# Kernel tuning notes

Measured on AMD Instinct MI355X. Metric: run time of the kernel, lower is better.

Reference implementation:

```python
import jax, jax.numpy as jnp
import numpy as np

N, K, C, G = 100000, 16, 64, 8
EPS = 1e-5


def bn(x, gamma, beta):
    # training-mode BatchNorm1d over all dims except channel (last)
    axes = tuple(range(x.ndim - 1))
    m = jnp.mean(x, axis=axes)
    v = jnp.var(x, axis=axes)
    return (x - m) * jax.lax.rsqrt(v + EPS) * gamma + beta


def setup_inputs() -> dict:
    key = jax.random.key(0)
    ks = jax.random.split(key, 16)

    def lin(k, i, o):
        return (jax.random.normal(k, (i, o), jnp.float32) / np.sqrt(i)).astype(jnp.float32)

    feat = jax.random.normal(ks[0], (N, C), jnp.float32)
    coord = jax.random.uniform(ks[1], (N, 3), jnp.float32) * 10.0
    ref = jax.random.randint(ks[2], (N, K), 0, N)
    drop = jax.random.uniform(ks[3], (N, K)) < 0.05  # some padded (-1) neighbors
    ref = jnp.where(drop, -1, ref)

    return {
        "feat": feat, "coord": coord, "reference_index": ref,
        "wq": lin(ks[4], C, C), "bq": jnp.zeros((C,), jnp.float32),
        "gq": jnp.ones((C,), jnp.float32), "betaq": jnp.zeros((C,), jnp.float32),
        "wk": lin(ks[5], C, C), "bk": jnp.zeros((C,), jnp.float32),
        "gk": jnp.ones((C,), jnp.float32), "betak": jnp.zeros((C,), jnp.float32),
        "wv": lin(ks[6], C, C), "bv": jnp.zeros((C,), jnp.float32),
        "wp1": lin(ks[7], 3, C), "bp1": jnp.zeros((C,), jnp.float32),
        "gp": jnp.ones((C,), jnp.float32), "betap": jnp.zeros((C,), jnp.float32),
        "wp2": lin(ks[8], C, C), "bp2": jnp.zeros((C,), jnp.float32),
        "ww1": lin(ks[9], C, G), "bw1": jnp.zeros((G,), jnp.float32),
        "gw": jnp.ones((G,), jnp.float32), "betaw": jnp.zeros((G,), jnp.float32),
        "ww2": lin(ks[10], G, G), "bw2": jnp.zeros((G,), jnp.float32),
    }


def reference(feat, coord, reference_index,
              wq, bq, gq, betaq,
              wk, bk, gk, betak,
              wv, bv,
              wp1, bp1, gp, betap,
              wp2, bp2,
              ww1, bw1, gw, betaw,
              ww2, bw2):
    # q/k/v projections
    q = jax.nn.relu(bn(feat @ wq + bq, gq, betaq))   # [N, C]
    k = jax.nn.relu(bn(feat @ wk + bk, gk, betak))   # [N, C]
    v = feat @ wv + bv                                # [N, C]

    idx = jnp.clip(reference_index, 0, N - 1)         # clipped gather index [N, K]
    mask = (reference_index >= 0).astype(feat.dtype)  # sign(ref + 1)

    key_n = k[idx]                                    # [N, K, C] neighbor keys
    val = v[idx]                                      # [N, K, C]
    pos = coord[idx] - coord[:, None, :]              # [N, K, 3] relative coords

    relation_qk = key_n - q[:, None, :]               # [N, K, C]

    # pe_bias branch
    peb = jax.nn.relu(bn(pos @ wp1 + bp1, gp, betap)) @ wp2 + bp2  # [N, K, C]
    relation_qk = relation_qk + peb
    val = val + peb

    # weight encoding -> grouped softmax over neighbors, masked
    w = jax.nn.relu(bn(relation_qk @ ww1 + bw1, gw, betaw)) @ ww2 + bw2  # [N, K, G]
    w = jax.nn.softmax(w, axis=1) * mask[:, :, None]

    val = val.reshape(N, K, G, C // G)
    out = jnp.einsum('nsgi,nsg->ngi', val, w).reshape(N, C)
    return out
```

## Files before the change

### kernel.cpp

```cpp
#include <hip/hip_runtime.h>
#include <hip/hip_bf16.h>

#define NPTS 100000
#define KNBR 16
#define CCH  64
#define GRP  8
#define BN_EPS 1e-5f
#define NROW (NPTS * KNBR)
#define NBATCH (NROW / 64)
#define NPB   ((NPTS + 63) / 64)

#define O_QLINH 0
#define O_KLINH (NPTS * 32)
#define O_VLINH (NPTS * 64)
#define O_STAT  (NPTS * 96)
#define O_AFF   (O_STAT + 416)
#define O_W2W1  (O_AFF + 416)
#define O_BW1E  (O_W2W1 + 512)
#define O_QW1   (O_BW1E + 8)
#define O_KW1   (O_QW1 + NPTS * 8)

typedef __attribute__((ext_vector_type(8))) short short8;
typedef __attribute__((ext_vector_type(4))) short short4v;
typedef __attribute__((ext_vector_type(4))) float f32x4;
#define MFMA16(a, b, c) __builtin_amdgcn_mfma_f32_16x16x32_bf16(a, b, c, 0, 0, 0)

__device__ __forceinline__ int clip_idx(int r) {
    int i = r < 0 ? 0 : r;
    return i >= NPTS ? NPTS - 1 : i;
}
__device__ __forceinline__ unsigned short f2bf(float x) {
    union { float f; unsigned u; } v; v.f = x;
    unsigned r = v.u + 0x7fffu + ((v.u >> 16) & 1u);
    return (unsigned short)(r >> 16);
}
__device__ __forceinline__ float bf2f(unsigned short h) {
    union { unsigned u; float f; } v; v.u = ((unsigned)h) << 16;
    return v.f;
}
__device__ __forceinline__ unsigned pk_bf16(float lo, float hi) {
    unsigned r;
    asm("v_cvt_pk_bf16_f32 %0, %1, %2" : "=v"(r) : "v"(lo), "v"(hi));
    return r;
}
__device__ __forceinline__ int physK(int s) {
    return (s >> 5) * 32 + ((s >> 2) & 3) * 8 + ((s >> 4) & 1) * 4 + (s & 3);
}
__device__ __forceinline__ int aOff(int r, int p) {
    return r * 64 + (((p >> 3) ^ (r & 7)) << 3) + (p & 7);
}
__device__ __forceinline__ int kib_of(int i, int q) {
    return (i < 4) ? (4 * q + i) : (16 + 4 * q + (i - 4));
}

__global__ __launch_bounds__(512) void k_prep(
    const float* __restrict__ wp2, const float* __restrict__ ww1,
    const float* __restrict__ bw1, const float* __restrict__ bp2,
    float* __restrict__ stat, float* __restrict__ w2w1, float* __restrict__ bw1e)
{
    int t = threadIdx.x;
    if (t < 416) stat[t] = 0.f;
    int j = t >> 3, g = t & 7;
    float acc = 0.f;
    #pragma unroll 16
    for (int c = 0; c < 64; ++c) acc = fmaf(wp2[j * 64 + c], ww1[c * 8 + g], acc);
    w2w1[t] = acc;
    if (t < 8) {
        float b = bw1[t];
        #pragma unroll 16
        for (int c = 0; c < 64; ++c) b = fmaf(bp2[c], ww1[c * 8 + t], b);
        bw1e[t] = b;
    }
}

#define QKV_BLOCKS 512
__global__ __launch_bounds__(256) void k_qkv(
    const float* __restrict__ feat,
    const float* __restrict__ wq, const float* __restrict__ bq,
    const float* __restrict__ wk, const float* __restrict__ bk,
    const float* __restrict__ wv, const float* __restrict__ bv,
    const float* __restrict__ bp2,
    const float* __restrict__ coord, const int* __restrict__ ref,
    short* __restrict__ QlinH, short* __restrict__ KlinH, short* __restrict__ VlinH,
    float* __restrict__ stat)
{
    __shared__ short sA[4096];
    __shared__ float s_red[9];
    const int tid = threadIdx.x, lane = tid & 63, w = tid >> 6;
    const int q = lane >> 4, c15 = lane & 15;

    if (blockIdx.x >= QKV_BLOCKS) {
        float m[9];
        #pragma unroll
        for (int i = 0; i < 9; ++i) m[i] = 0.f;
        const int gid = (blockIdx.x - QKV_BLOCKS) * 256 + tid;
        const int stride = 128 * 256;
        for (int row = gid; row < NROW; row += stride) {
            int n = row >> 4;
            int idx = clip_idx(ref[row]);
            float px = coord[idx * 3 + 0] - coord[n * 3 + 0];
            float py = coord[idx * 3 + 1] - coord[n * 3 + 1];
            float pz = coord[idx * 3 + 2] - coord[n * 3 + 2];
            m[0] += px; m[1] += py; m[2] += pz;
            m[3] = fmaf(px, px, m[3]); m[4] = fmaf(py, py, m[4]); m[5] = fmaf(pz, pz, m[5]);
            m[6] = fmaf(px, py, m[6]); m[7] = fmaf(px, pz, m[7]); m[8] = fmaf(py, pz, m[8]);
        }
        if (tid < 9) s_red[tid] = 0.f;
        __syncthreads();
        #pragma unroll
        for (int off = 32; off >= 1; off >>= 1) {
            #pragma unroll
            for (int i = 0; i < 9; ++i) m[i] += __shfl_xor(m[i], off, 64);
        }
        if (lane == 0) {
            #pragma unroll
            for (int i = 0; i < 9; ++i) atomicAdd(&s_red[i], m[i]);
        }
        __syncthreads();
        if (tid < 9) atomicAdd(&stat[256 + tid], s_red[tid]);
        return;
    }

    short8 bfrag[3][2];
    float bias[3];
    #pragma unroll
    for (int t = 0; t < 3; ++t) {
        int gt = w * 3 + t;
        const float* W = (gt < 4) ? wq : (gt < 8) ? wk : wv;
        const float* B = (gt < 4) ? bq : (gt < 8) ? bk : bv;
        int col = (gt * 16 + c15) & 63;
        bias[t] = B[col] + (gt >= 8 ? bp2[col] : 0.f);
        #pragma unroll
        for (int kt = 0; kt < 2; ++kt) {
            short8 bb;
            #pragma unroll
            for (int i = 0; i < 8; ++i) {
                int kk = kt * 32 + kib_of(i, q);
                bb[i] = (short)f2bf(W[kk * 64 + col]);
            }
            bfrag[t][kt] = bb;
        }
    }
    float st_s[3], st_q[3];
    #pragma unroll
    for (int t = 0; t < 3; ++t) { st_s[t] = 0.f; st_q[t] = 0.f; }

    const int c4 = c15 * 4;
    const int pk4 = physK(c4);

    for (int b = blockIdx.x; b < NPB; b += QKV_BLOCKS) {
        const int pbase = b * 64;
        #pragma unroll
        for (int i = 0; i < 4; ++i) {
            int p = w * 16 + i * 4 + q;
            int n = pbase + p;
            float4 v = make_float4(0.f, 0.f, 0.f, 0.f);
            if (n < NPTS) v = *(const float4*)(feat + n * 64 + c4);
            short4v h;
            h[0] = (short)f2bf(v.x); h[1] = (short)f2bf(v.y);
            h[2] = (short)f2bf(v.z); h[3] = (short)f2bf(v.w);
            *(short4v*)(sA + aOff(p, pk4)) = h;
        }
        __syncthreads();
        #pragma unroll
        for (int mt = 0; mt < 4; ++mt) {
            int r = mt * 16 + c15;
            int ch0 = q ^ (r & 7);
            int ch1 = (4 + q) ^ (r & 7);
            short8 a0 = *(const short8*)(sA + r * 64 + (ch0 << 3));
            short8 a1 = *(const short8*)(sA + r * 64 + (ch1 << 3));
            #pragma unroll
            for (int t = 0; t < 3; ++t) {
                f32x4 acc = (f32x4){0.f, 0.f, 0.f, 0.f};
                acc = MFMA16(a0, bfrag[t][0], acc);
                acc = MFMA16(a1, bfrag[t][1], acc);
                int gt = w * 3 + t;
                #pragma unroll
                for (int rg = 0; rg < 4; ++rg) {
                    int row = mt * 16 + 4 * q + rg;
                    int n = pbase + row;
                    if (n < NPTS) {
                        unsigned short h = f2bf(acc[rg] + bias[t]);
                        float vr = bf2f(h);
                        if (gt < 4)      QlinH[n * 64 + gt * 16 + c15] = (short)h;
                        else if (gt < 8) KlinH[n * 64 + (gt - 4) * 16 + c15] = (short)h;
                        else             VlinH[n * 64 + (gt - 8) * 16 + c15] = (short)h;
                        if (gt < 8) { st_s[t] += vr; st_q[t] = fmaf(vr, vr, st_q[t]); }
                    }
                }
            }
        }
        __syncthreads();
    }
    #pragma unroll
    for (int t = 0; t < 3; ++t) {
        st_s[t] += __shfl_xor(st_s[t], 16, 64); st_s[t] += __shfl_xor(st_s[t], 32, 64);
        st_q[t] += __shfl_xor(st_q[t], 16, 64); st_q[t] += __shfl_xor(st_q[t], 32, 64);
    }
    if (q == 0) {
        #pragma unroll
        for (int t = 0; t < 3; ++t) {
            int gt = w * 3 + t;
            if (gt < 4) {
                atomicAdd(&stat[gt * 16 + c15], st_s[t]);
                atomicAdd(&stat[64 + gt * 16 + c15], st_q[t]);
            } else if (gt < 8) {
                atomicAdd(&stat[128 + (gt - 4) * 16 + c15], st_s[t]);
                atomicAdd(&stat[192 + (gt - 4) * 16 + c15], st_q[t]);
            }
        }
    }
}

__global__ __launch_bounds__(192) void k_finA(
    const float* __restrict__ gq, const float* __restrict__ betaq,
    const float* __restrict__ gk, const float* __restrict__ betak,
    const float* __restrict__ gp, const float* __restrict__ betap,
    const float* __restrict__ wp1, const float* __restrict__ bp1,
    const float* __restrict__ stat, float* __restrict__ aff)
{
    int t = threadIdx.x;
    if (t < 64) {
        float m = stat[t] / (float)NPTS;
        float v = stat[64 + t] / (float)NPTS - m * m;
        float a = gq[t] * rsqrtf(v + BN_EPS);
        aff[t] = a;
        aff[64 + t] = betaq[t] - m * a;
    } else if (t < 128) {
        int c = t - 64;
        float m = stat[128 + c] / (float)NPTS;
        float v = stat[192 + c] / (float)NPTS - m * m;
        float a = gk[c] * rsqrtf(v + BN_EPS);
        aff[128 + c] = a;
        aff[192 + c] = betak[c] - m * a;
    } else {
        int c = t - 128;
        const float R = (float)NROW;
        float Ex = stat[256] / R, Ey = stat[257] / R, Ez = stat[258] / R;
        float Exx = stat[259] / R, Eyy = stat[260] / R, Ezz = stat[261] / R;
        float Exy = stat[262] / R, Exz = stat[263] / R, Eyz = stat[264] / R;
        float Cxx = Exx - Ex * Ex, Cyy = Eyy - Ey * Ey, Czz = Ezz - Ez * Ez;
        float Cxy = Exy - Ex * Ey, Cxz = Exz - Ex * Ez, Cyz = Eyz - Ey * Ez;
        float a0 = wp1[c], a1 = wp1[64 + c], a2 = wp1[128 + c];
        float mean = a0 * Ex + a1 * Ey + a2 * Ez + bp1[c];
        float var = a0 * a0 * Cxx + a1 * a1 * Cyy + a2 * a2 * Czz
                  + 2.f * (a0 * a1 * Cxy + a0 * a2 * Cxz + a1 * a2 * Cyz);
        float a = gp[c] * rsqrtf(var + BN_EPS);
        aff[256 + c] = a;
        aff[320 + c] = betap[c] - mean * a;
    }
}

__global__ __launch_bounds__(128) void k_qkw(
    const short* __restrict__ QlinH, const short* __restrict__ KlinH,
    const float* __restrict__ ww1, const float* __restrict__ aff,
    float* __restrict__ QW1, float* __restrict__ KW1)
{
    __shared__ short sA[2][8192];
    const int tid = threadIdx.x, lane = tid & 63, w = tid >> 6;
    const int q = lane >> 4, g = lane & 15;
    short8 bimg[2];
    #pragma unroll
    for (int kt = 0; kt < 2; ++kt) {
        short8 bb;
        #pragma unroll
        for (int i = 0; i < 8; ++i) {
            int s = kt * 32 + kib_of(i, q);
            bb[i] = (short)f2bf(g < 8 ? ww1[s * 8 + g] : 0.f);
        }
        bimg[kt] = bb;
    }
    const int r8 = lane >> 3, c8 = (lane & 7) * 8;
    f32x4 qa0 = *(const f32x4*)(aff + c8),       qa1 = *(const f32x4*)(aff + c8 + 4);
    f32x4 qb0 = *(const f32x4*)(aff + 64 + c8),  qb1 = *(const f32x4*)(aff + 64 + c8 + 4);
    f32x4 ka0 = *(const f32x4*)(aff + 128 + c8), ka1 = *(const f32x4*)(aff + 128 + c8 + 4);
    f32x4 kb0 = *(const f32x4*)(aff + 192 + c8), kb1 = *(const f32x4*)(aff + 192 + c8 + 4);
    const int pkA = physK(c8), pkB = physK(c8 + 4);
    short* AQ = sA[w];
    short* AK = sA[w] + 4096;

    for (int b = blockIdx.x * 2 + w; b < NPB; b += gridDim.x * 2) {
        const int pbase = b * 64;
        #pragma unroll
        for (int it = 0; it < 8; ++it) {
            int p = it * 8 + r8;
            int n = pbase + p;
            short8 qraw = {0,0,0,0,0,0,0,0}, kraw = {0,0,0,0,0,0,0,0};
            if (n < NPTS) {
                qraw = *(const short8*)(QlinH + n * 64 + c8);
                kraw = *(const short8*)(KlinH + n * 64 + c8);
            }
            float qf[8], kf[8];
            #pragma unroll
            for (int e = 0; e < 4; ++e) {
                qf[e]     = fmaxf(fmaf(bf2f((unsigned short)qraw[e]), qa0[e], qb0[e]), 0.f);
                qf[e + 4] = fmaxf(fmaf(bf2f((unsigned short)qraw[e + 4]), qa1[e], qb1[e]), 0.f);
                kf[e]     = fmaxf(fmaf(bf2f((unsigned short)kraw[e]), ka0[e], kb0[e]), 0.f);
                kf[e + 4] = fmaxf(fmaf(bf2f((unsigned short)kraw[e + 4]), ka1[e], kb1[e]), 0.f);
            }
            uint2 qv0 = make_uint2(pk_bf16(qf[0], qf[1]), pk_bf16(qf[2], qf[3]));
            uint2 qv1 = make_uint2(pk_bf16(qf[4], qf[5]), pk_bf16(qf[6], qf[7]));
            uint2 kv0 = make_uint2(pk_bf16(kf[0], kf[1]), pk_bf16(kf[2], kf[3]));
            uint2 kv1 = make_uint2(pk_bf16(kf[4], kf[5]), pk_bf16(kf[6], kf[7]));
            *(uint2*)(AQ + aOff(p, pkA)) = qv0;
            *(uint2*)(AQ + aOff(p, pkB)) = qv1;
            *(uint2*)(AK + aOff(p, pkA)) = kv0;
            *(uint2*)(AK + aOff(p, pkB)) = kv1;
        }
        #pragma unroll
        for (int mt = 0; mt < 4; ++mt) {
            f32x4 aq = (f32x4){0.f, 0.f, 0.f, 0.f};
            f32x4 ak = (f32x4){0.f, 0.f, 0.f, 0.f};
            int r = mt * 16 + g;
            #pragma unroll
            for (int kt = 0; kt < 2; ++kt) {
                int chunk = (kt * 4 + q) ^ (r & 7);
                aq = MFMA16(*(const short8*)(AQ + r * 64 + (chunk << 3)), bimg[kt], aq);
                ak = MFMA16(*(const short8*)(AK + r * 64 + (chunk << 3)), bimg[kt], ak);
            }
            if (g < 8) {
                #pragma unroll
                for (int rg = 0; rg < 4; ++rg) {
                    int n = pbase + mt * 16 + 4 * q + rg;
                    if (n < NPTS) {
                        QW1[n * 8 + g] = aq[rg];
                        KW1[n * 8 + g] = ak[rg];
                    }
                }
            }
        }
    }
}

__global__ __launch_bounds__(128) void k_wstats(
    const float* __restrict__ coord, const int* __restrict__ ref,
    const float* __restrict__ wp1, const float* __restrict__ bp1,
    const float* __restrict__ bw1e, const float* __restrict__ w2w1,
    const float* __restrict__ QW1, const float* __restrict__ KW1,
    const float* __restrict__ aff, float* __restrict__ stat)
{
    __shared__ short sP[2][4096];
    __shared__ float sPos[2][256];
    __shared__ int   sIdx[2][64];
    __shared__ float sRed[16];
    const int tid = threadIdx.x, lane = tid & 63, w = tid >> 6;
    const int q = lane >> 4, g = lane & 15, g7 = lane & 7;
    short8 bimg[2];
    #pragma unroll
    for (int kt = 0; kt < 2; ++kt) {
        short8 bb;
        #pragma unroll
        for (int i = 0; i < 8; ++i) {
            int s = kt * 32 + kib_of(i, q);
            bb[i] = (short)f2bf(g < 8 ? w2w1[s * 8 + g] : 0.f);
        }
        bimg[kt] = bb;
    }
    if (tid < 16) sRed[tid] = 0.f;
    __syncthreads();

    const int c2 = (lane & 31) * 2, rh5 = (lane >> 5) * 32;
    const float paL = aff[256 + c2],     paH = aff[256 + c2 + 1];
    const float A0L = paL * wp1[c2],       A0H = paH * wp1[c2 + 1];
    const float A1L = paL * wp1[64 + c2],  A1H = paH * wp1[64 + c2 + 1];
    const float A2L = paL * wp1[128 + c2], A2H = paH * wp1[128 + c2 + 1];
    const float B0L = fmaf(paL, bp1[c2], aff[320 + c2]);
    const float B0H = fmaf(paH, bp1[c2 + 1], aff[320 + c2 + 1]);
    const int pOff = physK(c2);
    const float bwg = bw1e[g7];

    short* P = sP[w];
    float* pos = sPos[w];
    int* idxs = sIdx[w];
    float accS = 0.f, accQ = 0.f;

    for (int b = blockIdx.x * 2 + w; b < NBATCH; b += gridDim.x * 2) {
        const int rbase = b * 64;
        const int p0 = b * 4;
        {
            int r = ref[rbase + lane];
            int idx = clip_idx(r);
            idxs[lane] = idx;
            int n = p0 + (lane >> 4);
            pos[lane * 4 + 0] = coord[idx * 3 + 0] - coord[n * 3 + 0];
            pos[lane * 4 + 1] = coord[idx * 3 + 1] - coord[n * 3 + 1];
            pos[lane * 4 + 2] = coord[idx * 3 + 2] - coord[n * 3 + 2];
        }
        float kwc[16], qwc[4];
        #pragma unroll
        for (int mt = 0; mt < 4; ++mt) {
            int4 i4 = *(const int4*)(idxs + mt * 16 + 4 * q);
            kwc[mt * 4 + 0] = KW1[i4.x * 8 + g7];
            kwc[mt * 4 + 1] = KW1[i4.y * 8 + g7];
            kwc[mt * 4 + 2] = KW1[i4.z * 8 + g7];
            kwc[mt * 4 + 3] = KW1[i4.w * 8 + g7];
            qwc[mt] = QW1[(p0 + mt) * 8 + g7];
        }
        #pragma unroll 8
        for (int rr = 0; rr < 32; ++rr) {
            int row = rh5 + rr;
            f32x4 pp = *(const f32x4*)(pos + row * 4);
            float lo = fmaxf(fmaf(pp.x, A0L, fmaf(pp.y, A1L, fmaf(pp.z, A2L, B0L))), 0.f);
            float hi = fmaxf(fmaf(pp.x, A0H, fmaf(pp.y, A1H, fmaf(pp.z, A2H, B0H))), 0.f);
            *(unsigned*)(P + aOff(row, pOff)) = pk_bf16(lo, hi);
        }
        #pragma unroll
        for (int mt = 0; mt < 4; ++mt) {
            f32x4 acc = (f32x4){0.f, 0.f, 0.f, 0.f};
            int r = mt * 16 + g;
            #pragma unroll
            for (int kt = 0; kt < 2; ++kt) {
                int chunk = (kt * 4 + q) ^ (r & 7);
                acc = MFMA16(*(const short8*)(P + r * 64 + (chunk << 3)), bimg[kt], acc);
            }
            if (g < 8) {
                float dq = bwg - qwc[mt];
                #pragma unroll
                for (int rg = 0; rg < 4; ++rg) {
                    float W = acc[rg] + kwc[mt * 4 + rg] + dq;
                    accS += W;
                    accQ = fmaf(W, W, accQ);
                }
            }
        }
    }
    accS += __shfl_xor(accS, 16, 64); accS += __shfl_xor(accS, 32, 64);
    accQ += __shfl_xor(accQ, 16, 64); accQ += __shfl_xor(accQ, 32, 64);
    if (lane < 8) {
        atomicAdd(&sRed[lane], accS);
        atomicAdd(&sRed[8 + lane], accQ);
    }
    __syncthreads();
    if (tid < 16) atomicAdd(&stat[384 + tid], sRed[tid]);
}

__global__ __launch_bounds__(64) void k_finB(
    const float* __restrict__ gw_, const float* __restrict__ betaw,
    const float* __restrict__ stat, float* __restrict__ aff)
{
    int t = threadIdx.x;
    if (t < 8) {
        const float M = (float)NROW;
        float m = stat[384 + t] / M;
        float v = stat[392 + t] / M - m * m;
        float a = gw_[t] * rsqrtf(v + BN_EPS);
        aff[384 + t] = a;
        aff[392 + t] = betaw[t] - m * a;
    }
}

__global__ __launch_bounds__(128) void k_final(
    const float* __restrict__ coord, const int* __restrict__ ref,
    const float* __restrict__ wp1, const float* __restrict__ bp1,
    const float* __restrict__ wp2,
    const float* __restrict__ bw1e, const float* __restrict__ w2w1,
    const float* __restrict__ ww2, const float* __restrict__ bw2,
    const float* __restrict__ QW1, const float* __restrict__ KW1,
    const short* __restrict__ VlinH,
    const float* __restrict__ aff, float* __restrict__ out)
{
    __shared__ short sP[2][4096];
    __shared__ float sPos[2][256];
    __shared__ int   sIdx[2][64];
    __shared__ float sWn[2][576];
    __shared__ float sW2[72];
    const int tid = threadIdx.x, lane = tid & 63, w = tid >> 6;
    const int q = lane >> 4, g15 = lane & 15, g7 = lane & 7;

    if (tid < 64) sW2[tid] = ww2[tid];
    else if (tid < 72) sW2[tid] = bw2[tid - 64];
    __syncthreads();

    short8 bw_img[2];
    #pragma unroll
    for (int kt = 0; kt < 2; ++kt) {
        short8 bb;
        #pragma unroll
        for (int i = 0; i < 8; ++i) {
            int s = kt * 32 + kib_of(i, q);
            bb[i] = (short)f2bf(g15 < 8 ? w2w1[s * 8 + g15] : 0.f);
        }
        bw_img[kt] = bb;
    }
    short8 b1[8];
    #pragma unroll
    for (int tt = 0; tt < 8; ++tt) {
        int kt = tt & 1, nt = tt >> 1;
        short8 bb;
        #pragma unroll
        for (int i = 0; i < 8; ++i) {
            int kk = kt * 32 + kib_of(i, q);
            bb[i] = (short)f2bf(wp2[kk * 64 + nt * 16 + g15]);
        }
        b1[tt] = bb;
    }

    const int c2 = (lane & 31) * 2, rh5 = (lane >> 5) * 32;
    const float paL = aff[256 + c2],     paH = aff[256 + c2 + 1];
    const float A0L = paL * wp1[c2],       A0H = paH * wp1[c2 + 1];
    const float A1L = paL * wp1[64 + c2],  A1H = paH * wp1[64 + c2 + 1];
    const float A2L = paL * wp1[128 + c2], A2H = paH * wp1[128 + c2 + 1];
    const float B0L = fmaf(paL, bp1[c2], aff[320 + c2]);
    const float B0H = fmaf(paH, bp1[c2 + 1], aff[320 + c2 + 1]);
    const int pOff = physK(c2);
    const float bwg = bw1e[g7];
    const float wag = aff[384 + g7], wbg = aff[392 + g7];

    short* P = sP[w];
    float* pos = sPos[w];
    int* idxs = sIdx[w];
    float* wn = sWn[w];

#define LOADV(MT, VC) do {                                              \
        int4 i4_ = *(const int4*)(idxs + (MT) * 16 + 4 * q);            \
        int ia_[4] = {i4_.x, i4_.y, i4_.z, i4_.w};                      \
        _Pragma("unroll")                                               \
        for (int rg = 0; rg < 4; ++rg) {                                \
            const short* vb_ = VlinH + ia_[rg] * 64 + g15;              \
            _Pragma("unroll")                                           \
            for (int nt = 0; nt < 4; ++nt)                              \
                VC[rg * 4 + nt] = (unsigned short)vb_[nt * 16];         \
        }                                                               \
    } while (0)

#define EINSUM_MT(MT, VC) do {                                          \
        int r_ = (MT) * 16 + g15;                                       \
        int c0_ = q ^ (r_ & 7);                                         \
        int c1_ = (4 + q) ^ (r_ & 7);                                   \
        short8 a0_ = *(const short8*)(P + r_ * 64 + (c0_ << 3));        \
        short8 a1_ = *(const short8*)(P + r_ * 64 + (c1_ << 3));        \
        const int ro0_ = ((MT) * 16 + 4 * q) * 9;                       \
        _Pragma("unroll")                                               \
        for (int nt = 0; nt < 4; ++nt) {                                \
            f32x4 acc_ = (f32x4){0.f, 0.f, 0.f, 0.f};                   \
            acc_ = MFMA16(a0_, b1[nt * 2 + 0], acc_);                   \
            acc_ = MFMA16(a1_, b1[nt * 2 + 1], acc_);                   \
            int col_ = nt * 16 + g15;                                   \
            int o_ = nt * 2 + (g15 >> 3);                               \
            float part_ = 0.f;                                          \
            _Pragma("unroll")                                           \
            for (int rg = 0; rg < 4; ++rg) {                            \
                float v_ = bf2f(VC[rg * 4 + nt]);                       \
                part_ = fmaf(v_ + acc_[rg], wn[ro0_ + rg * 9 + o_], part_); \
            }                                                           \
            part_ += __shfl_xor(part_, 16, 64);                         \
            part_ += __shfl_xor(part_, 32, 64);                         \
            if (q == 0) out[(p0 + (MT)) * 64 + col_] = part_;           \
        }                                                               \
    } while (0)

    for (int b = blockIdx.x * 2 + w; b < NBATCH; b += gridDim.x * 2) {
        const int rbase = b * 64;
        const int p0 = b * 4;
        {
            int r = ref[rbase + lane];
            int idx = clip_idx(r);
            idxs[lane] = idx;
            int n = p0 + (lane >> 4);
            pos[lane * 4 + 0] = coord[idx * 3 + 0] - coord[n * 3 + 0];
            pos[lane * 4 + 1] = coord[idx * 3 + 1] - coord[n * 3 + 1];
            pos[lane * 4 + 2] = coord[idx * 3 + 2] - coord[n * 3 + 2];
            pos[lane * 4 + 3] = (r >= 0) ? 1.f : 0.f;
        }
        float kwc[16], qwc[4];
        #pragma unroll
        for (int mt = 0; mt < 4; ++mt) {
            int4 i4 = *(const int4*)(idxs + mt * 16 + 4 * q);
            kwc[mt * 4 + 0] = KW1[i4.x * 8 + g7];
            kwc[mt * 4 + 1] = KW1[i4.y * 8 + g7];
            kwc[mt * 4 + 2] = KW1[i4.z * 8 + g7];
            kwc[mt * 4 + 3] = KW1[i4.w * 8 + g7];
            qwc[mt] = QW1[(p0 + mt) * 8 + g7];
        }
        unsigned short vcA[16], vcB[16], vcC[16], vcD[16];
        LOADV(0, vcA);
        LOADV(1, vcB);
        #pragma unroll 8
        for (int rr = 0; rr < 32; ++rr) {
            int row = rh5 + rr;
            f32x4 pp = *(const f32x4*)(pos + row * 4);
            float lo = fmaxf(fmaf(pp.x, A0L, fmaf(pp.y, A1L, fmaf(pp.z, A2L, B0L))), 0.f);
            float hi = fmaxf(fmaf(pp.x, A0H, fmaf(pp.y, A1H, fmaf(pp.z, A2H, B0H))), 0.f);
            *(unsigned*)(P + aOff(row, pOff)) = pk_bf16(lo, hi);
        }
        #pragma unroll
        for (int mt = 0; mt < 4; ++mt) {
            f32x4 acc = (f32x4){0.f, 0.f, 0.f, 0.f};
            int r = mt * 16 + g15;
            #pragma unroll
            for (int kt = 0; kt < 2; ++kt) {
                int chunk = (kt * 4 + q) ^ (r & 7);
                acc = MFMA16(*(const short8*)(P + r * 64 + (chunk << 3)), bw_img[kt], acc);
            }
            if (g15 < 8) {
                float dq = bwg - qwc[mt];
                #pragma unroll
                for (int rg = 0; rg < 4; ++rg) {
                    int row = mt * 16 + 4 * q + rg;
                    float W = acc[rg] + kwc[mt * 4 + rg] + dq;
                    wn[row * 9 + g15] = fmaxf(fmaf(wag, W, wbg), 0.f);
                }
            }
        }
        LOADV(2, vcC);
        LOADV(3, vcD);
        {
            float h[8];
            #pragma unroll
            for (int gg = 0; gg < 8; ++gg) h[gg] = wn[lane * 9 + gg];
            float mask = pos[lane * 4 + 3];
            #pragma unroll
            for (int o = 0; o < 8; ++o) {
                float acc = sW2[64 + o];
                #pragma unroll
                for (int gg = 0; gg < 8; ++gg) acc = fmaf(h[gg], sW2[gg * 8 + o], acc);
                float e = __expf(acc);
                float s = e;
                s += __shfl_xor(s, 1, 64);
                s += __shfl_xor(s, 2, 64);
                s += __shfl_xor(s, 4, 64);
                s += __shfl_xor(s, 8, 64);
                wn[lane * 9 + o] = e * __builtin_amdgcn_rcpf(s) * mask;
            }
        }
        EINSUM_MT(0, vcA);
        EINSUM_MT(1, vcB);
        EINSUM_MT(2, vcC);
        EINSUM_MT(3, vcD);
    }
#undef LOADV
#undef EINSUM_MT
}

extern "C" void kernel_launch(void* const* d_in, const int* in_sizes, int n_in,
                              void* d_out, int out_size, void* d_ws, size_t ws_size,
                              hipStream_t stream)
{
    const float* feat  = (const float*)d_in[0];
    const float* coord = (const float*)d_in[1];
    const int*   ref   = (const int*)d_in[2];
    const float* wq    = (const float*)d_in[3];
    const float* bq    = (const float*)d_in[4];
    const float* gq    = (const float*)d_in[5];
    const float* betaq = (const float*)d_in[6];
    const float* wk    = (const float*)d_in[7];
    const float* bk    = (const float*)d_in[8];
    const float* gk    = (const float*)d_in[9];
    const float* betak = (const float*)d_in[10];
    const float* wv    = (const float*)d_in[11];
    const float* bv    = (const float*)d_in[12];
    const float* wp1   = (const float*)d_in[13];
    const float* bp1   = (const float*)d_in[14];
    const float* gp    = (const float*)d_in[15];
    const float* betap = (const float*)d_in[16];
    const float* wp2   = (const float*)d_in[17];
    const float* bp2   = (const float*)d_in[18];
    const float* ww1   = (const float*)d_in[19];
    const float* bw1   = (const float*)d_in[20];
    const float* gw_   = (const float*)d_in[21];
    const float* betaw = (const float*)d_in[22];
    const float* ww2   = (const float*)d_in[23];
    const float* bw2   = (const float*)d_in[24];

    float* ws    = (float*)d_ws;
    short* QlinH = (short*)(ws + O_QLINH);
    short* KlinH = (short*)(ws + O_KLINH);
    short* VlinH = (short*)(ws + O_VLINH);
    float* stat  = ws + O_STAT;
    float* aff   = ws + O_AFF;
    float* w2w1  = ws + O_W2W1;
    float* bw1e  = ws + O_BW1E;
    float* QW1   = ws + O_QW1;
    float* KW1   = ws + O_KW1;
    float* out   = (float*)d_out;

    hipLaunchKernelGGL(k_prep, dim3(1), dim3(512), 0, stream,
                       wp2, ww1, bw1, bp2, stat, w2w1, bw1e);
    hipLaunchKernelGGL(k_qkv, dim3(QKV_BLOCKS + 128), dim3(256), 0, stream,
                       feat, wq, bq, wk, bk, wv, bv, bp2, coord, ref,
                       QlinH, KlinH, VlinH, stat);
    hipLaunchKernelGGL(k_finA, dim3(1), dim3(192), 0, stream,
                       gq, betaq, gk, betak, gp, betap, wp1, bp1, stat, aff);
    hipLaunchKernelGGL(k_qkw, dim3(782), dim3(128), 0, stream,
                       QlinH, KlinH, ww1, aff, QW1, KW1);
    hipLaunchKernelGGL(k_wstats, dim3(2500), dim3(128), 0, stream,
                       coord, ref, wp1, bp1, bw1e, w2w1, QW1, KW1, aff, stat);
    hipLaunchKernelGGL(k_finB, dim3(1), dim3(64), 0, stream, gw_, betaw, stat, aff);
    hipLaunchKernelGGL(k_final, dim3(2500), dim3(128), 0, stream,
                       coord, ref, wp1, bp1, wp2, bw1e, w2w1, ww2, bw2,
                       QW1, KW1, VlinH, aff, out);
}
```

Before: 220.7 us.

## Materialize pre-BN weight logits in bf16 during stats pass, reuse in final

The stats kernel now writes each row's 8 pre-BN weight-encoding values as bf16 to a workspace buffer, and computes the BN statistics from the rounded values so they stay consistent. The final kernel reads these values with one 16-byte load per row instead of gathering KW1/QW1 and recomputing the small MFMA product. This removes redundant gathers and MFMA work in the final pass, at the cost of about 25.6 MB of extra global writes and reads, plus bf16 rounding of the logits.

```diff
diff --git a/kernel.cpp b/kernel.cpp
--- a/kernel.cpp
+++ b/kernel.cpp
@@ -19,6 +19,7 @@
 #define O_BW1E  (O_W2W1 + 512)
 #define O_QW1   (O_BW1E + 8)
 #define O_KW1   (O_QW1 + NPTS * 8)
+#define O_W1H   (O_KW1 + NPTS * 8)
 
 typedef __attribute__((ext_vector_type(8))) short short8;
 typedef __attribute__((ext_vector_type(4))) short short4v;
@@ -337,7 +338,8 @@
     const float* __restrict__ wp1, const float* __restrict__ bp1,
     const float* __restrict__ bw1e, const float* __restrict__ w2w1,
     const float* __restrict__ QW1, const float* __restrict__ KW1,
-    const float* __restrict__ aff, float* __restrict__ stat)
+    const float* __restrict__ aff, float* __restrict__ stat,
+    short* __restrict__ W1H)
 {
     __shared__ short sP[2][4096];
     __shared__ float sPos[2][256];
@@ -417,9 +419,12 @@
                 float dq = bwg - qwc[mt];
                 #pragma unroll
                 for (int rg = 0; rg < 4; ++rg) {
-                    float W = acc[rg] + kwc[mt * 4 + rg] + dq;
-                    accS += W;
-                    accQ = fmaf(W, W, accQ);
+                    float Wf = acc[rg] + kwc[mt * 4 + rg] + dq;
+                    unsigned short wh = f2bf(Wf);
+                    float Wr = bf2f(wh);
+                    accS += Wr;
+                    accQ = fmaf(Wr, Wr, accQ);
+                    W1H[(rbase + mt * 16 + 4 * q + rg) * 8 + g7] = (short)wh;
                 }
             }
         }
@@ -453,10 +458,8 @@
     const float* __restrict__ coord, const int* __restrict__ ref,
     const float* __restrict__ wp1, const float* __restrict__ bp1,
     const float* __restrict__ wp2,
-    const float* __restrict__ bw1e, const float* __restrict__ w2w1,
     const float* __restrict__ ww2, const float* __restrict__ bw2,
-    const float* __restrict__ QW1, const float* __restrict__ KW1,
-    const short* __restrict__ VlinH,
+    const short* __restrict__ W1H, const short* __restrict__ VlinH,
     const float* __restrict__ aff, float* __restrict__ out)
 {
     __shared__ short sP[2][4096];
@@ -465,23 +468,12 @@
     __shared__ float sWn[2][576];
     __shared__ float sW2[72];
     const int tid = threadIdx.x, lane = tid & 63, w = tid >> 6;
-    const int q = lane >> 4, g15 = lane & 15, g7 = lane & 7;
+    const int q = lane >> 4, g15 = lane & 15;
 
     if (tid < 64) sW2[tid] = ww2[tid];
     else if (tid < 72) sW2[tid] = bw2[tid - 64];
     __syncthreads();
 
-    short8 bw_img[2];
-    #pragma unroll
-    for (int kt = 0; kt < 2; ++kt) {
-        short8 bb;
-        #pragma unroll
-        for (int i = 0; i < 8; ++i) {
-            int s = kt * 32 + kib_of(i, q);
-            bb[i] = (short)f2bf(g15 < 8 ? w2w1[s * 8 + g15] : 0.f);
-        }
-        bw_img[kt] = bb;
-    }
     short8 b1[8];
     #pragma unroll
     for (int tt = 0; tt < 8; ++tt) {
@@ -503,8 +495,12 @@
     const float B0L = fmaf(paL, bp1[c2], aff[320 + c2]);
     const float B0H = fmaf(paH, bp1[c2 + 1], aff[320 + c2 + 1]);
     const int pOff = physK(c2);
-    const float bwg = bw1e[g7];
-    const float wag = aff[384 + g7], wbg = aff[392 + g7];
+    float wa8[8], wb8[8];
+    #pragma unroll
+    for (int gg = 0; gg < 8; ++gg) {
+        wa8[gg] = aff[384 + gg];
+        wb8[gg] = aff[392 + gg];
+    }
 
     short* P = sP[w];
     float* pos = sPos[w];
@@ -562,16 +558,7 @@
             pos[lane * 4 + 2] = coord[idx * 3 + 2] - coord[n * 3 + 2];
             pos[lane * 4 + 3] = (r >= 0) ? 1.f : 0.f;
         }
-        float kwc[16], qwc[4];
-        #pragma unroll
-        for (int mt = 0; mt < 4; ++mt) {
-            int4 i4 = *(const int4*)(idxs + mt * 16 + 4 * q);
-            kwc[mt * 4 + 0] = KW1[i4.x * 8 + g7];
-            kwc[mt * 4 + 1] = KW1[i4.y * 8 + g7];
-            kwc[mt * 4 + 2] = KW1[i4.z * 8 + g7];
-            kwc[mt * 4 + 3] = KW1[i4.w * 8 + g7];
-            qwc[mt] = QW1[(p0 + mt) * 8 + g7];
-        }
+        short8 w8 = *(const short8*)(W1H + (rbase + lane) * 8);
         unsigned short vcA[16], vcB[16], vcC[16], vcD[16];
         LOADV(0, vcA);
         LOADV(1, vcB);
@@ -583,31 +570,15 @@
             float hi = fmaxf(fmaf(pp.x, A0H, fmaf(pp.y, A1H, fmaf(pp.z, A2H, B0H))), 0.f);
             *(unsigned*)(P + aOff(row, pOff)) = pk_bf16(lo, hi);
         }
-        #pragma unroll
-        for (int mt = 0; mt < 4; ++mt) {
-            f32x4 acc = (f32x4){0.f, 0.f, 0.f, 0.f};
-            int r = mt * 16 + g15;
-            #pragma unroll
-            for (int kt = 0; kt < 2; ++kt) {
-                int chunk = (kt * 4 + q) ^ (r & 7);
-                acc = MFMA16(*(const short8*)(P + r * 64 + (chunk << 3)), bw_img[kt], acc);
-            }
-            if (g15 < 8) {
-                float dq = bwg - qwc[mt];
-                #pragma unroll
-                for (int rg = 0; rg < 4; ++rg) {
-                    int row = mt * 16 + 4 * q + rg;
-                    float W = acc[rg] + kwc[mt * 4 + rg] + dq;
-                    wn[row * 9 + g15] = fmaxf(fmaf(wag, W, wbg), 0.f);
-                }
-            }
-        }
         LOADV(2, vcC);
         LOADV(3, vcD);
         {
             float h[8];
             #pragma unroll
-            for (int gg = 0; gg < 8; ++gg) h[gg] = wn[lane * 9 + gg];
+            for (int gg = 0; gg < 8; ++gg) {
+                float Wf = bf2f((unsigned short)w8[gg]);
+                h[gg] = fmaxf(fmaf(wa8[gg], Wf, wb8[gg]), 0.f);
+            }
             float mask = pos[lane * 4 + 3];
             #pragma unroll
             for (int o = 0; o < 8; ++o) {
@@ -672,6 +643,7 @@
     float* bw1e  = ws + O_BW1E;
     float* QW1   = ws + O_QW1;
     float* KW1   = ws + O_KW1;
+    short* W1H   = (short*)(ws + O_W1H);
     float* out   = (float*)d_out;
 
     hipLaunchKernelGGL(k_prep, dim3(1), dim3(512), 0, stream,
@@ -684,9 +656,9 @@
     hipLaunchKernelGGL(k_qkw, dim3(782), dim3(128), 0, stream,
                        QlinH, KlinH, ww1, aff, QW1, KW1);
     hipLaunchKernelGGL(k_wstats, dim3(2500), dim3(128), 0, stream,
-                       coord, ref, wp1, bp1, bw1e, w2w1, QW1, KW1, aff, stat);
+                       coord, ref, wp1, bp1, bw1e, w2w1, QW1, KW1, aff, stat, W1H);
     hipLaunchKernelGGL(k_finB, dim3(1), dim3(64), 0, stream, gw_, betaw, stat, aff);
     hipLaunchKernelGGL(k_final, dim3(2500), dim3(128), 0, stream,
-                       coord, ref, wp1, bp1, wp2, bw1e, w2w1, ww2, bw2,
-                       QW1, KW1, VlinH, aff, out);
-}
+                       coord, ref, wp1, bp1, wp2, ww2, bw2,
+                       W1H, VlinH, aff, out);
+}
```

Result: faster. 215.4 us (-2.4%).
